# Optimization experiments

Measured on AMD Instinct MI355X. Metric: run time of the kernel, lower is better.

## Reference

```python
import jax, jax.numpy as jnp
import numpy as np

B, S, D = 1, 2048, 2048
H, KVH, HD = 32, 8, 64
FFN = 8192
N_EXPERTS, TOP_K = 32, 4
EPS = 1e-5
NEG = -1e9


def setup_inputs() -> dict:
    key = jax.random.key(0)
    ks = jax.random.split(key, 24)
    s = 0.02
    inp = {}
    inp['hidden_states'] = jax.random.normal(ks[0], (B, S, D), jnp.float32)
    # RoPE tables: cos/sin of shape [B, S, HD]
    inv_freq = 1.0 / (10000.0 ** (np.arange(0, HD, 2, dtype=np.float32) / HD))
    t = np.arange(S, dtype=np.float32)
    freqs = np.outer(t, inv_freq)                      # [S, HD/2]
    emb = np.concatenate([freqs, freqs], axis=-1)      # [S, HD]
    inp['cos'] = jnp.asarray(np.cos(emb))[None].repeat(B, axis=0)
    inp['sin'] = jnp.asarray(np.sin(emb))[None].repeat(B, axis=0)
    # additive causal mask [B, 1, S, S]
    causal = jnp.where(jnp.tril(jnp.ones((S, S), bool)), 0.0, NEG).astype(jnp.float32)
    inp['attention_mask'] = jnp.broadcast_to(causal[None, None], (B, 1, S, S))
    # attention params
    inp['wq'] = jax.random.normal(ks[1], (H * HD, D), jnp.float32) * s
    inp['bq'] = jnp.zeros((H * HD,), jnp.float32)
    inp['wk'] = jax.random.normal(ks[2], (KVH * HD, D), jnp.float32) * s
    inp['bk'] = jnp.zeros((KVH * HD,), jnp.float32)
    inp['wv'] = jax.random.normal(ks[3], (KVH * HD, D), jnp.float32) * s
    inp['bv'] = jnp.zeros((KVH * HD,), jnp.float32)
    inp['wo'] = jax.random.normal(ks[4], (D, H * HD), jnp.float32) * s
    inp['bo'] = jnp.zeros((D,), jnp.float32)
    # norms
    inp['ln1_w'] = jnp.ones((D,), jnp.float32)
    inp['ln2_w'] = jnp.ones((D,), jnp.float32)
    # MoE gate + shared expert MLP
    inp['gate_w'] = jax.random.normal(ks[5], (N_EXPERTS, D), jnp.float32) * s
    inp['gate_b'] = jnp.zeros((N_EXPERTS,), jnp.float32)
    inp['w1'] = jax.random.normal(ks[6], (FFN, D), jnp.float32) * s
    inp['b1'] = jnp.zeros((FFN,), jnp.float32)
    inp['w2'] = jax.random.normal(ks[7], (D, FFN), jnp.float32) * s
    inp['b2'] = jnp.zeros((D,), jnp.float32)
    inp['w3'] = jax.random.normal(ks[8], (FFN, D), jnp.float32) * s
    inp['b3'] = jnp.zeros((FFN,), jnp.float32)
    return inp


def _rms_norm(x, w, eps=EPS):
    x32 = x.astype(jnp.float32)
    var = jnp.mean(x32 * x32, axis=-1, keepdims=True)
    return (w * (x32 * jax.lax.rsqrt(var + eps))).astype(x.dtype)


def _rotate_half(x):
    x1, x2 = jnp.split(x, 2, axis=-1)
    return jnp.concatenate([-x2, x1], axis=-1)


def _decoder_layer(hidden_states, cos, sin, attention_mask,
                   wq, bq, wk, bk, wv, bv, wo, bo, ln1_w, ln2_w,
                   gate_w, gate_b, w1, b1, w2, b2, w3, b3):
    residual = hidden_states
    x = _rms_norm(hidden_states, ln1_w)

    # projections -> [B, heads, S, HD]
    q = (x @ wq.T + bq).reshape(B, S, H, HD).transpose(0, 2, 1, 3)
    k = (x @ wk.T + bk).reshape(B, S, KVH, HD).transpose(0, 2, 1, 3)
    v = (x @ wv.T + bv).reshape(B, S, KVH, HD).transpose(0, 2, 1, 3)

    # RoPE (cos/sin unsqueezed on head dim)
    c, s_ = cos[:, None], sin[:, None]
    q = q * c + _rotate_half(q) * s_
    k = k * c + _rotate_half(k) * s_

    # GQA: repeat kv heads
    n_rep = H // KVH
    k = jnp.repeat(k, n_rep, axis=1)
    v = jnp.repeat(v, n_rep, axis=1)

    scaling = HD ** -0.5
    scores = jnp.einsum('bhqd,bhkd->bhqk', q, k) * scaling + attention_mask
    probs = jax.nn.softmax(scores.astype(jnp.float32), axis=-1).astype(q.dtype)
    attn = jnp.einsum('bhqk,bhkd->bhqd', probs, v)
    attn = attn.transpose(0, 2, 1, 3).reshape(B, S, H * HD)
    attn = attn @ wo.T + bo

    hidden_states = residual + attn
    residual = hidden_states
    x = _rms_norm(hidden_states, ln2_w)

    # MoE block (as written in source: router computed, but ALL tokens go
    # through one shared expert MLP; routing weights unused in output)
    flat = x.reshape(-1, D)
    router_logits = flat @ gate_w.T + gate_b                     # [B*S, E]
    rw = jax.nn.softmax(router_logits.astype(jnp.float32), axis=-1)
    rw_top, sel = jax.lax.top_k(rw, TOP_K)                       # computed, unused
    del rw_top, sel

    h1 = flat @ w1.T + b1
    h3 = flat @ w3.T + b3
    mlp = (jax.nn.silu(h1) * h3) @ w2.T + b2
    hidden_states = residual + mlp.reshape(B, S, D)
    return hidden_states


def reference(hidden_states, cos, sin, attention_mask,
              wq, bq, wk, bk, wv, bv, wo, bo, ln1_w, ln2_w,
              gate_w, gate_b, w1, b1, w2, b2, w3, b3):
    return _decoder_layer(hidden_states, cos, sin, attention_mask,
                          wq, bq, wk, bk, wv, bv, wo, bo, ln1_w, ln2_w,
                          gate_w, gate_b, w1, b1, w2, b2, w3, b3)
```

## Files before the change

kernel.cpp:

```cpp
#include <hip/hip_runtime.h>

#define S_LEN 2048
#define DMODEL 2048
#define NH 32
#define NKV 8
#define HD 64
#define FFN_DIM 8192

typedef __attribute__((ext_vector_type(4))) float f32x4;
typedef __attribute__((ext_vector_type(16))) float f32x16;
typedef __attribute__((ext_vector_type(8))) short bf16x8;

#define MFMA(a, b, c) __builtin_amdgcn_mfma_f32_16x16x32_bf16(a, b, c, 0, 0, 0)
#define MFMA32(a, b, c) __builtin_amdgcn_mfma_f32_32x32x16_bf16(a, b, c, 0, 0, 0)

__device__ __forceinline__ ushort f2bf(float f) {
  unsigned u = __float_as_uint(f);
  unsigned r = (u + 0x7fffu + ((u >> 16) & 1u)) >> 16;
  return (ushort)r;
}
__device__ __forceinline__ float bf2f(ushort s) {
  return __uint_as_float(((unsigned)s) << 16);
}
__device__ __forceinline__ unsigned cvtpk(float a, float b) {
  unsigned r;
  asm("v_cvt_pk_bf16_f32 %0, %1, %2" : "=v"(r) : "v"(a), "v"(b));
  return r;
}

__device__ __forceinline__ void gload16(const void* g, void* l) {
  __builtin_amdgcn_global_load_lds(
      (const __attribute__((address_space(1))) void*)g,
      (__attribute__((address_space(3))) void*)l, 16, 0, 0);
}

__device__ __forceinline__ void phase_bar() {
  asm volatile("" ::: "memory");
  __builtin_amdgcn_sched_barrier(0);
  __builtin_amdgcn_s_barrier();
  __builtin_amdgcn_sched_barrier(0);
  asm volatile("" ::: "memory");
}

__global__ __launch_bounds__(256) void cvt_k(const float* __restrict__ in,
                                             ushort* __restrict__ out) {
  int i = blockIdx.x * 256 + threadIdx.x;
  f32x4 a = ((const f32x4*)in)[i * 2];
  f32x4 b = ((const f32x4*)in)[i * 2 + 1];
  bf16x8 r;
#pragma unroll
  for (int j = 0; j < 4; j++) r[j] = (short)f2bf(a[j]);
#pragma unroll
  for (int j = 0; j < 4; j++) r[4 + j] = (short)f2bf(b[j]);
  ((bf16x8*)out)[i] = r;
}

__global__ __launch_bounds__(256) void bias3_k(const float* __restrict__ a,
                                               const float* __restrict__ b,
                                               const float* __restrict__ c,
                                               float* __restrict__ out) {
  int i = blockIdx.x * 256 + threadIdx.x;
  float v;
  if (i < 2048) v = a[i];
  else if (i < 2560) v = b[i - 2048];
  else v = c[i - 2560];
  out[i] = v;
}

__global__ __launch_bounds__(256) void rmsnorm_k(const float* __restrict__ in,
                                                 const float* __restrict__ w,
                                                 ushort* __restrict__ out) {
  const int row = blockIdx.x;
  const int tid = threadIdx.x;
  const float* x = in + (size_t)row * DMODEL;
  f32x4 v0 = *(const f32x4*)(x + tid * 8);
  f32x4 v1 = *(const f32x4*)(x + tid * 8 + 4);
  float ss = v0[0] * v0[0] + v0[1] * v0[1] + v0[2] * v0[2] + v0[3] * v0[3] +
             v1[0] * v1[0] + v1[1] * v1[1] + v1[2] * v1[2] + v1[3] * v1[3];
#pragma unroll
  for (int off = 32; off; off >>= 1) ss += __shfl_xor(ss, off, 64);
  __shared__ float red[4];
  if ((tid & 63) == 0) red[tid >> 6] = ss;
  __syncthreads();
  float tot = red[0] + red[1] + red[2] + red[3];
  float inv = rsqrtf(tot * (1.f / DMODEL) + 1e-5f);
#pragma unroll
  for (int i = 0; i < 8; i++) {
    int c = tid * 8 + i;
    float val = (i < 4) ? v0[i] : v1[i - 4];
    out[(size_t)row * DMODEL + c] = f2bf(w[c] * val * inv);
  }
}

__global__ __launch_bounds__(256) void rope_k(ushort* __restrict__ qkv,
                                              const float* __restrict__ cs,
                                              const float* __restrict__ sn) {
  int idx = blockIdx.x * 256 + threadIdx.x;
  int d = idx & 31;
  int t = idx >> 5;
  int head = t % (NH + NKV);
  int s = t / (NH + NKV);
  int col = (head < NH) ? head * HD : DMODEL + (head - NH) * HD;
  ushort* p = qkv + (size_t)s * 3072 + col;
  float lo = bf2f(p[d]), hi = bf2f(p[d + 32]);
  float c = cs[s * HD + d], si = sn[s * HD + d];
  p[d] = f2bf(lo * c - hi * si);
  p[d + 32] = f2bf(hi * c + lo * si);
}

enum { EPI_BF16 = 0, EPI_RESID = 1, EPI_SILU = 2, EPI_MUL = 3, EPI_PART = 4 };

__device__ __forceinline__ void quad(const bf16x8* Arr, const bf16x8* BR,
                                     f32x4 (*accr)[4], int qn) {
#pragma unroll
  for (int i = 0; i < 4; i++)
#pragma unroll
    for (int j = 0; j < 2; j++)
#pragma unroll
      for (int ks = 0; ks < 2; ks++)
        accr[i][qn * 2 + j] =
            MFMA(Arr[2 * i + ks], BR[2 * j + ks], accr[i][qn * 2 + j]);
}

template <int EPI>
__global__ __launch_bounds__(512, 2) void gemm256(
    const ushort* __restrict__ A, int lda, const ushort* __restrict__ B,
    int ldb, const float* __restrict__ bias, const float* __restrict__ resid,
    ushort* __restrict__ outb, float* __restrict__ outf, int ldc, int K,
    int kspan, long long opart) {
  __shared__ __align__(16) ushort lds[65536];
  const int tid = threadIdx.x;
  const int l = tid & 63, w = tid >> 6;
  const int g = l >> 4, r16 = l & 15;
  const int wm = w >> 2, wn = w & 3;

  int nwg = gridDim.x * gridDim.y;
  int bid = blockIdx.y * gridDim.x + blockIdx.x;
  bid = (bid & 7) * (nwg >> 3) + (bid >> 3);
  const int m0 = (bid % gridDim.x) * 256;
  const int n0 = (bid / gridDim.x) * 256;
  const int z = blockIdx.z;

  const ushort* Ag = A + (size_t)z * kspan + (size_t)m0 * lda;
  const ushort* Bg = B + (size_t)z * kspan + (size_t)n0 * ldb;
  ushort* outbz = outb;
  if (EPI == EPI_PART) outbz = outb + (size_t)z * opart;

  const int NT = K >> 6;

  const int stgRow = w * 8 + (l >> 3);
  const int stgCol = ((l & 7) ^ (l >> 3)) * 8;

  const int xa = (r16 & 7) << 4;
  const int c0 = ((g * 16) ^ xa) >> 1;
  const int c1 = c0 ^ 32;
  const int slotA = wm ? 3 : 1;
  const int slotB = (wn >> 1) ? 2 : 0;
  const ushort* pA0 = lds + slotA * 8192 + r16 * 64 + c0;
  const ushort* pA1 = lds + slotA * 8192 + r16 * 64 + c1;
  const ushort* pB0 = lds + slotB * 8192 + ((wn & 1) * 64 + r16) * 64 + c0;
  const ushort* pB1 = lds + slotB * 8192 + ((wn & 1) * 64 + r16) * 64 + c1;

  f32x4 acc[8][4];
#pragma unroll
  for (int i = 0; i < 8; i++)
#pragma unroll
    for (int j = 0; j < 4; j++) acc[i][j] = (f32x4){0, 0, 0, 0};

  auto stageA = [&](int slot, int tile, int hf) {
    ushort* dst = lds + ((tile & 1) * 32768 + slot * 8192 + w * 512);
    const ushort* src =
        Ag + (size_t)(hf * 128 + stgRow) * lda + tile * 64 + stgCol;
    gload16(src, dst);
    gload16(src + (size_t)64 * lda, dst + 4096);
  };
  auto stageB = [&](int slot, int tile, int hf) {
    ushort* dst = lds + ((tile & 1) * 32768 + slot * 8192 + w * 512);
    const ushort* src =
        Bg + (size_t)(hf * 128 + stgRow) * ldb + tile * 64 + stgCol;
    gload16(src, dst);
    gload16(src + (size_t)64 * ldb, dst + 4096);
  };

  stageB(0, 0, 0);
  stageA(1, 0, 0);
  stageB(2, 0, 1);
  stageA(3, 0, 1);
  stageB(0, 1, 0);
  stageA(1, 1, 0);
  asm volatile("s_waitcnt vmcnt(4)" ::: "memory");
  phase_bar();

  bf16x8 Ar[8], Br0[4], Br1[4];

  for (int t = 0; t < NT; ++t) {
    const int bo = (t & 1) * 32768;
#pragma unroll
    for (int i = 0; i < 4; i++) {
      Ar[2 * i] = *(const bf16x8*)(pA0 + bo + i * 1024);
      Ar[2 * i + 1] = *(const bf16x8*)(pA1 + bo + i * 1024);
    }
#pragma unroll
    for (int j = 0; j < 2; j++) {
      Br0[2 * j] = *(const bf16x8*)(pB0 + bo + j * 1024);
      Br0[2 * j + 1] = *(const bf16x8*)(pB1 + bo + j * 1024);
    }
    if (t + 1 < NT) stageB(2, t + 1, 1);
    phase_bar();
    __builtin_amdgcn_s_setprio(1);
    quad(Ar, Br0, &acc[0], 0);
    __builtin_amdgcn_s_setprio(0);
    phase_bar();
#pragma unroll
    for (int j = 0; j < 2; j++) {
      Br1[2 * j] = *(const bf16x8*)(pB0 + bo + (j + 2) * 1024);
      Br1[2 * j + 1] = *(const bf16x8*)(pB1 + bo + (j + 2) * 1024);
    }
    if (t + 1 < NT) stageA(3, t + 1, 1);
    phase_bar();
    __builtin_amdgcn_s_setprio(1);
    quad(Ar, Br1, &acc[0], 1);
    __builtin_amdgcn_s_setprio(0);
    phase_bar();
#pragma unroll
    for (int i = 0; i < 4; i++) {
      Ar[2 * i] = *(const bf16x8*)(pA0 + bo + (i + 4) * 1024);
      Ar[2 * i + 1] = *(const bf16x8*)(pA1 + bo + (i + 4) * 1024);
    }
    if (t + 2 < NT) stageB(0, t + 2, 0);
    phase_bar();
    __builtin_amdgcn_s_setprio(1);
    quad(Ar, Br1, &acc[4], 1);
    __builtin_amdgcn_s_setprio(0);
    phase_bar();
    if (t + 2 < NT) stageA(1, t + 2, 0);
    phase_bar();
    __builtin_amdgcn_s_setprio(1);
    quad(Ar, Br0, &acc[4], 0);
    __builtin_amdgcn_s_setprio(0);
    if (t + 2 < NT) {
      asm volatile("s_waitcnt vmcnt(4)" ::: "memory");
    } else {
      asm volatile("s_waitcnt vmcnt(0)" ::: "memory");
    }
    phase_bar();
  }

#pragma unroll
  for (int mf = 0; mf < 8; mf++) {
#pragma unroll
    for (int nf = 0; nf < 4; nf++) {
      const int n = n0 + wn * 64 + nf * 16 + r16;
      float bia = (EPI == EPI_PART) ? 0.f : bias[n];
#pragma unroll
      for (int reg = 0; reg < 4; reg++) {
        const int m = m0 + wm * 128 + mf * 16 + g * 4 + reg;
        float v = acc[mf][nf][reg] + bia;
        if constexpr (EPI == EPI_BF16) {
          outbz[(size_t)m * ldc + n] = f2bf(v);
        } else if constexpr (EPI == EPI_RESID) {
          outf[(size_t)m * ldc + n] = v + resid[(size_t)m * ldc + n];
        } else if constexpr (EPI == EPI_SILU) {
          float sv = v / (1.f + __expf(-v));
          outbz[(size_t)m * ldc + n] = f2bf(sv);
        } else if constexpr (EPI == EPI_MUL) {
          float hv = bf2f(outbz[(size_t)m * ldc + n]);
          outbz[(size_t)m * ldc + n] = f2bf(v * hv);
        } else {
          outbz[(size_t)m * ldc + n] = f2bf(v);
        }
      }
    }
  }
}

__global__ __launch_bounds__(256) void reduce_k(const ushort* __restrict__ part,
                                                const float* __restrict__ b2,
                                                float* __restrict__ out) {
  int i = (blockIdx.x * 256 + threadIdx.x) * 8;
  int col = i & (DMODEL - 1);
  float s[8];
#pragma unroll
  for (int j = 0; j < 8; j++) s[j] = out[i + j] + b2[col + j];
#pragma unroll
  for (int z = 0; z < 4; z++) {
    bf16x8 v = *(const bf16x8*)(part + (size_t)z * 4194304 + i);
#pragma unroll
    for (int j = 0; j < 8; j++) s[j] += bf2f((ushort)v[j]);
  }
#pragma unroll
  for (int j = 0; j < 8; j++) out[i + j] = s[j];
}

__global__ __launch_bounds__(256, 3) void flash2_k(const ushort* __restrict__ qkv,
                                                   ushort* __restrict__ att) {
  const int bid = blockIdx.x;
  const int head = (bid >> 4) & 31;
  const int rmap = bid & 15;
  const int qb = (bid & 256) ? (15 - rmap) : rmap;
  const int kvh = head >> 2;
  const int tid = threadIdx.x;
  const int w = tid >> 6, l = tid & 63;
  const int h = l >> 5, q31 = l & 31;
  const int qw = qb * 128 + w * 32;
  const int qrow = qw + q31;

  __shared__ __align__(16) ushort lds[2][8192];

  bf16x8 qreg[4];
  {
    const ushort* qp = qkv + (size_t)qrow * 3072 + head * HD;
#pragma unroll
    for (int s = 0; s < 4; s++)
      qreg[s] = *(const bf16x8*)(qp + s * 16 + h * 8);
  }

  f32x16 oacc[2];
#pragma unroll
  for (int i = 0; i < 16; i++) { oacc[0][i] = 0.f; oacc[1][i] = 0.f; }
  float mreg = -1e30f, lsum = 0.f;

  const int nt = 2 * qb + 2;

  const int skv = tid >> 2;
  const int sch = (tid & 3) * 2;
  const int vkv = tid & 63;
  const int vd0 = (tid >> 6) * 16;

  const ushort* kg_base = qkv + DMODEL + kvh * HD;

  bf16x8 krA, krB, vrA, vrB;
  auto loadTile = [&](int jb) {
    const ushort* kg = kg_base + (size_t)jb * 64 * 3072;
    krA = *(const bf16x8*)(kg + (size_t)skv * 3072 + sch * 8);
    krB = *(const bf16x8*)(kg + (size_t)skv * 3072 + sch * 8 + 8);
    const ushort* vg = kg + 512;
    vrA = *(const bf16x8*)(vg + (size_t)vkv * 3072 + vd0);
    vrB = *(const bf16x8*)(vg + (size_t)vkv * 3072 + vd0 + 8);
  };
  auto writeTile = [&](int b) {
    ushort* kb = lds[b];
    *(bf16x8*)(kb + skv * 64 + ((sch ^ (skv & 7)) * 8)) = krA;
    *(bf16x8*)(kb + skv * 64 + (((sch + 1) ^ (skv & 7)) * 8)) = krB;
    ushort* vb = lds[b] + 4096;
#pragma unroll
    for (int i = 0; i < 8; i++) {
      int d = vd0 + i;
      vb[d * 64 + (((vkv >> 3) ^ (d & 7)) * 8) + (vkv & 7)] = (ushort)vrA[i];
    }
#pragma unroll
    for (int i = 0; i < 8; i++) {
      int d = vd0 + 8 + i;
      vb[d * 64 + (((vkv >> 3) ^ (d & 7)) * 8) + (vkv & 7)] = (ushort)vrB[i];
    }
  };

  loadTile(0);
  for (int jb = 0; jb < nt; ++jb) {
    const int b = jb & 1;
    writeTile(b);
    __syncthreads();
    if (jb + 1 < nt) loadTile(jb + 1);

    if (jb * 64 <= qw + 31) {
      const ushort* Kb = lds[b];
      const ushort* Vb = lds[b] + 4096;

      f32x16 sacc[2];
#pragma unroll
      for (int i = 0; i < 16; i++) { sacc[0][i] = 0.f; sacc[1][i] = 0.f; }
#pragma unroll
      for (int c = 0; c < 2; c++) {
        const int kvr = c * 32 + q31;
        const ushort* kp = Kb + kvr * 64;
        const int kx = kvr & 7;
#pragma unroll
        for (int s = 0; s < 4; s++) {
          bf16x8 kf = *(const bf16x8*)(kp + ((2 * s + h) ^ kx) * 8);
          sacc[c] = MFMA32(kf, qreg[s], sacc[c]);
        }
      }

      const bool diag = (jb * 64 + 63 > qw);
      if (diag) {
#pragma unroll
        for (int c = 0; c < 2; c++)
#pragma unroll
          for (int rg = 0; rg < 16; rg++) {
            int kvg = jb * 64 + c * 32 + (rg & 3) + 8 * (rg >> 2) + 4 * h;
            if (kvg > qrow) sacc[c][rg] = -1e30f;
          }
      }
      float tmax = sacc[0][0];
#pragma unroll
      for (int rg = 1; rg < 16; rg++) tmax = fmaxf(tmax, sacc[0][rg]);
#pragma unroll
      for (int rg = 0; rg < 16; rg++) tmax = fmaxf(tmax, sacc[1][rg]);
      tmax = fmaxf(tmax, __shfl_xor(tmax, 32));
      const float mn = fmaxf(mreg, tmax);
      const float resc = __expf((mreg - mn) * 0.125f);
      mreg = mn;
      float rsum = 0.f;
#pragma unroll
      for (int c = 0; c < 2; c++)
#pragma unroll
        for (int rg = 0; rg < 16; rg++) {
          float pv = __expf((sacc[c][rg] - mn) * 0.125f);
          sacc[c][rg] = pv;
          rsum += pv;
        }
      rsum += __shfl_xor(rsum, 32);
      lsum = lsum * resc + rsum;
      oacc[0] *= resc;
      oacc[1] *= resc;

      unsigned pw_[2][4][2];
#pragma unroll
      for (int c = 0; c < 2; c++)
#pragma unroll
        for (int rr = 0; rr < 4; rr++) {
          pw_[c][rr][0] = cvtpk(sacc[c][4 * rr + 0], sacc[c][4 * rr + 1]);
          pw_[c][rr][1] = cvtpk(sacc[c][4 * rr + 2], sacc[c][4 * rr + 3]);
        }

#pragma unroll
      for (int s = 0; s < 4; s++) {
        const int c = s >> 1, base = (s & 1) * 2;
        unsigned k0 = h ? pw_[c][base + 1][0] : pw_[c][base][0];
        unsigned k1 = h ? pw_[c][base + 1][1] : pw_[c][base][1];
        unsigned s0 = h ? pw_[c][base][0] : pw_[c][base + 1][0];
        unsigned s1 = h ? pw_[c][base][1] : pw_[c][base + 1][1];
        unsigned t0 = __shfl_xor(s0, 32);
        unsigned t1 = __shfl_xor(s1, 32);
        union { unsigned u[4]; bf16x8 v; } pf;
        pf.u[0] = h ? t0 : k0;
        pf.u[1] = h ? t1 : k1;
        pf.u[2] = h ? k0 : t0;
        pf.u[3] = h ? k1 : t1;
#pragma unroll
        for (int dt = 0; dt < 2; dt++) {
          const int d = dt * 32 + q31;
          bf16x8 vf =
              *(const bf16x8*)(Vb + d * 64 + ((2 * s + h) ^ (d & 7)) * 8);
          oacc[dt] = MFMA32(vf, pf.v, oacc[dt]);
        }
      }
    }
  }

  const float inv = 1.f / lsum;
  ushort* op = att + (size_t)qrow * DMODEL + head * HD;
#pragma unroll
  for (int dt = 0; dt < 2; dt++)
#pragma unroll
    for (int rr = 0; rr < 4; rr++) {
      const int d0 = dt * 32 + 8 * rr + 4 * h;
      unsigned lo = cvtpk(oacc[dt][4 * rr + 0] * inv, oacc[dt][4 * rr + 1] * inv);
      unsigned hi = cvtpk(oacc[dt][4 * rr + 2] * inv, oacc[dt][4 * rr + 3] * inv);
      uint2 v2;
      v2.x = lo;
      v2.y = hi;
      *(uint2*)(op + d0) = v2;
    }
}

extern "C" void kernel_launch(void* const* d_in, const int* in_sizes, int n_in,
                              void* d_out, int out_size, void* d_ws,
                              size_t ws_size, hipStream_t stream) {
  (void)in_sizes; (void)n_in; (void)out_size; (void)ws_size;
  const float* hidden = (const float*)d_in[0];
  const float* cosb = (const float*)d_in[1];
  const float* sinb = (const float*)d_in[2];
  const float* wq = (const float*)d_in[4];
  const float* bq = (const float*)d_in[5];
  const float* wk = (const float*)d_in[6];
  const float* bk = (const float*)d_in[7];
  const float* wv = (const float*)d_in[8];
  const float* bv = (const float*)d_in[9];
  const float* wo = (const float*)d_in[10];
  const float* bo = (const float*)d_in[11];
  const float* ln1 = (const float*)d_in[12];
  const float* ln2 = (const float*)d_in[13];
  const float* w1 = (const float*)d_in[16];
  const float* b1 = (const float*)d_in[17];
  const float* w2 = (const float*)d_in[18];
  const float* b2 = (const float*)d_in[19];
  const float* w3 = (const float*)d_in[20];
  const float* b3 = (const float*)d_in[21];
  float* out = (float*)d_out;

  char* ws = (char*)d_ws;
  ushort* part = (ushort*)ws;
  ushort* x1 = (ushort*)ws;   ws += (size_t)S_LEN * DMODEL * 2;
  ushort* qkv = (ushort*)ws;  ws += (size_t)S_LEN * 3072 * 2;
  ushort* att = (ushort*)ws;  ws += (size_t)S_LEN * DMODEL * 2;
  ushort* x2 = (ushort*)ws;   ws += (size_t)S_LEN * DMODEL * 2;
  ushort* hbuf = (ushort*)ws; ws += (size_t)S_LEN * FFN_DIM * 2;
  ushort* wbuf = (ushort*)ws; ws += (size_t)FFN_DIM * DMODEL * 2;
  float* bqkv = (float*)ws;   ws += 3072 * 4;

  rmsnorm_k<<<S_LEN, 256, 0, stream>>>(hidden, ln1, x1);

  cvt_k<<<(2048 * 2048) / 2048, 256, 0, stream>>>(wq, wbuf);
  cvt_k<<<(512 * 2048) / 2048, 256, 0, stream>>>(wk, wbuf + 2048 * 2048);
  cvt_k<<<(512 * 2048) / 2048, 256, 0, stream>>>(wv, wbuf + 2560 * 2048);
  bias3_k<<<12, 256, 0, stream>>>(bq, bk, bv, bqkv);

  gemm256<EPI_BF16><<<dim3(8, 12), 512, 0, stream>>>(
      x1, DMODEL, wbuf, DMODEL, bqkv, nullptr, qkv, nullptr, 3072, DMODEL, 0,
      0);

  rope_k<<<(S_LEN * (NH + NKV) * 32) / 256, 256, 0, stream>>>(qkv, cosb, sinb);

  flash2_k<<<512, 256, 0, stream>>>(qkv, att);

  cvt_k<<<(2048 * 2048) / 2048, 256, 0, stream>>>(wo, wbuf);
  gemm256<EPI_RESID><<<dim3(8, 8), 512, 0, stream>>>(
      att, DMODEL, wbuf, DMODEL, bo, hidden, nullptr, out, DMODEL, DMODEL, 0,
      0);

  rmsnorm_k<<<S_LEN, 256, 0, stream>>>(out, ln2, x2);

  cvt_k<<<(FFN_DIM * 2048) / 2048, 256, 0, stream>>>(w1, wbuf);
  gemm256<EPI_SILU><<<dim3(8, 32), 512, 0, stream>>>(
      x2, DMODEL, wbuf, DMODEL, b1, nullptr, hbuf, nullptr, FFN_DIM, DMODEL, 0,
      0);

  cvt_k<<<(FFN_DIM * 2048) / 2048, 256, 0, stream>>>(w3, wbuf);
  gemm256<EPI_MUL><<<dim3(8, 32), 512, 0, stream>>>(
      x2, DMODEL, wbuf, DMODEL, b3, nullptr, hbuf, nullptr, FFN_DIM, DMODEL, 0,
      0);

  cvt_k<<<(DMODEL * FFN_DIM) / 2048, 256, 0, stream>>>(w2, wbuf);
  gemm256<EPI_PART><<<dim3(8, 8, 4), 512, 0, stream>>>(
      hbuf, FFN_DIM, wbuf, FFN_DIM, nullptr, nullptr, part, nullptr, DMODEL,
      DMODEL, DMODEL, (long long)S_LEN * DMODEL);
  reduce_k<<<(S_LEN * DMODEL) / 2048, 256, 0, stream>>>(part, b2, out);
}
```

Before: 462.3 us.

## Split-K the QKV and output-projection GEMMs and add generic partial reduce

The QKV projection now runs as a 2-way split-K GEMM and the output projection as a 4-way split-K GEMM. Their bf16 partials are summed by a templated reduce kernel that adds the bias and either the residual or a bf16 conversion. This raises the number of workgroups for GEMMs that previously launched too few tiles (96 and 64) to fill the GPU. The cost is extra partial writes and reads, plus rounding the partials to bf16. Separately, the three QKV weight conversions are merged into one launch, and the GEMM phase barriers drop their sched_barrier and memory clobbers in favour of a plain s_barrier.

```diff
diff --git a/kernel.cpp b/kernel.cpp
--- a/kernel.cpp
+++ b/kernel.cpp
@@ -34,14 +34,6 @@
       (__attribute__((address_space(3))) void*)l, 16, 0, 0);
 }
 
-__device__ __forceinline__ void phase_bar() {
-  asm volatile("" ::: "memory");
-  __builtin_amdgcn_sched_barrier(0);
-  __builtin_amdgcn_s_barrier();
-  __builtin_amdgcn_sched_barrier(0);
-  asm volatile("" ::: "memory");
-}
-
 __global__ __launch_bounds__(256) void cvt_k(const float* __restrict__ in,
                                              ushort* __restrict__ out) {
   int i = blockIdx.x * 256 + threadIdx.x;
@@ -53,6 +45,26 @@
 #pragma unroll
   for (int j = 0; j < 4; j++) r[4 + j] = (short)f2bf(b[j]);
   ((bf16x8*)out)[i] = r;
+}
+
+__global__ __launch_bounds__(256) void cvt_qkv_k(const float* __restrict__ wq,
+                                                 const float* __restrict__ wk,
+                                                 const float* __restrict__ wv,
+                                                 ushort* __restrict__ dst) {
+  int row = blockIdx.x;
+  const float* src;
+  if (row < 2048) src = wq + (size_t)row * DMODEL;
+  else if (row < 2560) src = wk + (size_t)(row - 2048) * DMODEL;
+  else src = wv + (size_t)(row - 2560) * DMODEL;
+  int i = threadIdx.x * 8;
+  f32x4 a = *(const f32x4*)(src + i);
+  f32x4 b = *(const f32x4*)(src + i + 4);
+  bf16x8 r;
+#pragma unroll
+  for (int j = 0; j < 4; j++) r[j] = (short)f2bf(a[j]);
+#pragma unroll
+  for (int j = 0; j < 4; j++) r[4 + j] = (short)f2bf(b[j]);
+  *(bf16x8*)(dst + (size_t)row * DMODEL + i) = r;
 }
 
 __global__ __launch_bounds__(256) void bias3_k(const float* __restrict__ a,
@@ -189,7 +201,7 @@
   stageB(0, 1, 0);
   stageA(1, 1, 0);
   asm volatile("s_waitcnt vmcnt(4)" ::: "memory");
-  phase_bar();
+  __builtin_amdgcn_s_barrier();
 
   bf16x8 Ar[8], Br0[4], Br1[4];
 
@@ -206,35 +218,35 @@
       Br0[2 * j + 1] = *(const bf16x8*)(pB1 + bo + j * 1024);
     }
     if (t + 1 < NT) stageB(2, t + 1, 1);
-    phase_bar();
+    __builtin_amdgcn_s_barrier();
     __builtin_amdgcn_s_setprio(1);
     quad(Ar, Br0, &acc[0], 0);
     __builtin_amdgcn_s_setprio(0);
-    phase_bar();
+    __builtin_amdgcn_s_barrier();
 #pragma unroll
     for (int j = 0; j < 2; j++) {
       Br1[2 * j] = *(const bf16x8*)(pB0 + bo + (j + 2) * 1024);
       Br1[2 * j + 1] = *(const bf16x8*)(pB1 + bo + (j + 2) * 1024);
     }
     if (t + 1 < NT) stageA(3, t + 1, 1);
-    phase_bar();
+    __builtin_amdgcn_s_barrier();
     __builtin_amdgcn_s_setprio(1);
     quad(Ar, Br1, &acc[0], 1);
     __builtin_amdgcn_s_setprio(0);
-    phase_bar();
+    __builtin_amdgcn_s_barrier();
 #pragma unroll
     for (int i = 0; i < 4; i++) {
       Ar[2 * i] = *(const bf16x8*)(pA0 + bo + (i + 4) * 1024);
       Ar[2 * i + 1] = *(const bf16x8*)(pA1 + bo + (i + 4) * 1024);
     }
     if (t + 2 < NT) stageB(0, t + 2, 0);
-    phase_bar();
+    __builtin_amdgcn_s_barrier();
     __builtin_amdgcn_s_setprio(1);
     quad(Ar, Br1, &acc[4], 1);
     __builtin_amdgcn_s_setprio(0);
-    phase_bar();
+    __builtin_amdgcn_s_barrier();
     if (t + 2 < NT) stageA(1, t + 2, 0);
-    phase_bar();
+    __builtin_amdgcn_s_barrier();
     __builtin_amdgcn_s_setprio(1);
     quad(Ar, Br0, &acc[4], 0);
     __builtin_amdgcn_s_setprio(0);
@@ -243,7 +255,7 @@
     } else {
       asm volatile("s_waitcnt vmcnt(0)" ::: "memory");
     }
-    phase_bar();
+    __builtin_amdgcn_s_barrier();
   }
 
 #pragma unroll
@@ -274,22 +286,30 @@
   }
 }
 
-__global__ __launch_bounds__(256) void reduce_k(const ushort* __restrict__ part,
-                                                const float* __restrict__ b2,
-                                                float* __restrict__ out) {
-  int i = (blockIdx.x * 256 + threadIdx.x) * 8;
-  int col = i & (DMODEL - 1);
+template <int MODE>
+__global__ __launch_bounds__(256) void reduce2_k(
+    const ushort* __restrict__ part, long long pstride, int nz,
+    const float* __restrict__ bias, int ncol, const float* __restrict__ resid,
+    float* __restrict__ outf, ushort* __restrict__ outb) {
+  long long i = (long long)(blockIdx.x * 256 + threadIdx.x) * 8;
+  int col = (int)(i % ncol);
   float s[8];
 #pragma unroll
-  for (int j = 0; j < 8; j++) s[j] = out[i + j] + b2[col + j];
-#pragma unroll
-  for (int z = 0; z < 4; z++) {
-    bf16x8 v = *(const bf16x8*)(part + (size_t)z * 4194304 + i);
+  for (int j = 0; j < 8; j++) s[j] = bias[col + j];
+  for (int zz = 0; zz < nz; zz++) {
+    bf16x8 v = *(const bf16x8*)(part + zz * pstride + i);
 #pragma unroll
     for (int j = 0; j < 8; j++) s[j] += bf2f((ushort)v[j]);
   }
-#pragma unroll
-  for (int j = 0; j < 8; j++) out[i + j] = s[j];
+  if constexpr (MODE == 1) {
+#pragma unroll
+    for (int j = 0; j < 8; j++) outf[i + j] = s[j] + resid[i + j];
+  } else {
+    bf16x8 r;
+#pragma unroll
+    for (int j = 0; j < 8; j++) r[j] = (short)f2bf(s[j]);
+    *(bf16x8*)(outb + i) = r;
+  }
 }
 
 __global__ __launch_bounds__(256, 3) void flash2_k(const ushort* __restrict__ qkv,
@@ -490,7 +510,6 @@
   float* out = (float*)d_out;
 
   char* ws = (char*)d_ws;
-  ushort* part = (ushort*)ws;
   ushort* x1 = (ushort*)ws;   ws += (size_t)S_LEN * DMODEL * 2;
   ushort* qkv = (ushort*)ws;  ws += (size_t)S_LEN * 3072 * 2;
   ushort* att = (ushort*)ws;  ws += (size_t)S_LEN * DMODEL * 2;
@@ -499,25 +518,31 @@
   ushort* wbuf = (ushort*)ws; ws += (size_t)FFN_DIM * DMODEL * 2;
   float* bqkv = (float*)ws;   ws += 3072 * 4;
 
+  ushort* partQ = att;
+  ushort* partO = x2;
+  ushort* partW = x1;
+
   rmsnorm_k<<<S_LEN, 256, 0, stream>>>(hidden, ln1, x1);
 
-  cvt_k<<<(2048 * 2048) / 2048, 256, 0, stream>>>(wq, wbuf);
-  cvt_k<<<(512 * 2048) / 2048, 256, 0, stream>>>(wk, wbuf + 2048 * 2048);
-  cvt_k<<<(512 * 2048) / 2048, 256, 0, stream>>>(wv, wbuf + 2560 * 2048);
+  cvt_qkv_k<<<3072, 256, 0, stream>>>(wq, wk, wv, wbuf);
   bias3_k<<<12, 256, 0, stream>>>(bq, bk, bv, bqkv);
 
-  gemm256<EPI_BF16><<<dim3(8, 12), 512, 0, stream>>>(
-      x1, DMODEL, wbuf, DMODEL, bqkv, nullptr, qkv, nullptr, 3072, DMODEL, 0,
-      0);
+  gemm256<EPI_PART><<<dim3(8, 12, 2), 512, 0, stream>>>(
+      x1, DMODEL, wbuf, DMODEL, nullptr, nullptr, partQ, nullptr, 3072, 1024,
+      1024, (long long)S_LEN * 3072);
+  reduce2_k<0><<<(S_LEN * 3072) / 2048, 256, 0, stream>>>(
+      partQ, (long long)S_LEN * 3072, 2, bqkv, 3072, nullptr, nullptr, qkv);
 
   rope_k<<<(S_LEN * (NH + NKV) * 32) / 256, 256, 0, stream>>>(qkv, cosb, sinb);
 
   flash2_k<<<512, 256, 0, stream>>>(qkv, att);
 
   cvt_k<<<(2048 * 2048) / 2048, 256, 0, stream>>>(wo, wbuf);
-  gemm256<EPI_RESID><<<dim3(8, 8), 512, 0, stream>>>(
-      att, DMODEL, wbuf, DMODEL, bo, hidden, nullptr, out, DMODEL, DMODEL, 0,
-      0);
+  gemm256<EPI_PART><<<dim3(8, 8, 4), 512, 0, stream>>>(
+      att, DMODEL, wbuf, DMODEL, nullptr, nullptr, partO, nullptr, DMODEL, 512,
+      512, (long long)S_LEN * DMODEL);
+  reduce2_k<1><<<(S_LEN * DMODEL) / 2048, 256, 0, stream>>>(
+      partO, (long long)S_LEN * DMODEL, 4, bo, DMODEL, hidden, out, nullptr);
 
   rmsnorm_k<<<S_LEN, 256, 0, stream>>>(out, ln2, x2);
 
@@ -533,7 +558,8 @@
 
   cvt_k<<<(DMODEL * FFN_DIM) / 2048, 256, 0, stream>>>(w2, wbuf);
   gemm256<EPI_PART><<<dim3(8, 8, 4), 512, 0, stream>>>(
-      hbuf, FFN_DIM, wbuf, FFN_DIM, nullptr, nullptr, part, nullptr, DMODEL,
+      hbuf, FFN_DIM, wbuf, FFN_DIM, nullptr, nullptr, partW, nullptr, DMODEL,
       DMODEL, DMODEL, (long long)S_LEN * DMODEL);
-  reduce_k<<<(S_LEN * DMODEL) / 2048, 256, 0, stream>>>(part, b2, out);
-}
+  reduce2_k<1><<<(S_LEN * DMODEL) / 2048, 256, 0, stream>>>(
+      partW, (long long)S_LEN * DMODEL, 4, b2, DMODEL, out, out, nullptr);
+}
```

Result: faster. 425.3 us (-8.0%).
